# Kernel optimization log

Measured on AMD Instinct MI355X. Metric: run time of the kernel, lower is better.

The kernel has to match this reference:

```python
import jax, jax.numpy as jnp
import numpy as np

B, T, H, V, ADIM, AMAX = 16, 1024, 512, 32000, 512, 10


def setup_inputs() -> dict:
    key = jax.random.key(0)
    ks = jax.random.split(key, 24)
    def n(k, shape, s=0.05):
        return jax.random.normal(k, shape, jnp.float32) * s
    return {
        "instruction": jax.random.randint(ks[0], (B, T), 0, V, dtype=jnp.int32),
        "emb": n(ks[1], (V, H)),
        "wih_f": n(ks[2], (4 * H, H)), "whh_f": n(ks[3], (4 * H, H)),
        "bih_f": n(ks[4], (4 * H,)), "bhh_f": n(ks[5], (4 * H,)),
        "wih_b": n(ks[6], (4 * H, H)), "whh_b": n(ks[7], (4 * H, H)),
        "bih_b": n(ks[8], (4 * H,)), "bhh_b": n(ks[9], (4 * H,)),
        "wg": n(ks[10], (2 * H, 2 * H)), "bg": n(ks[11], (2 * H,)),
        "ws1": n(ks[12], (H, 2 * H)), "bs1": n(ks[13], (H,)),
        "ws2": n(ks[14], (1, H)), "bs2": n(ks[15], (1,)),
        "wd1": n(ks[16], (H, 2 * H)), "bd1": n(ks[17], (H,)),
        "wd2": n(ks[18], (ADIM, H)), "bd2": n(ks[19], (ADIM,)),
        "max_actions": AMAX,
    }


def _lstm(x, wih, whh, bias):
    # x: [B, T, H] -> outputs [B, T, H]; PyTorch gate order i, f, g, o
    h0 = jnp.zeros((x.shape[0], whh.shape[1]), x.dtype)
    def step(carry, xt):
        h, c = carry
        g = xt @ wih.T + h @ whh.T + bias
        i, f, gg, o = jnp.split(g, 4, axis=-1)
        c = jax.nn.sigmoid(f) * c + jax.nn.sigmoid(i) * jnp.tanh(gg)
        h = jax.nn.sigmoid(o) * jnp.tanh(c)
        return (h, c), h
    _, hs = jax.lax.scan(step, (h0, h0), jnp.swapaxes(x, 0, 1))
    return jnp.swapaxes(hs, 0, 1)


def reference(instruction, emb, wih_f, whh_f, bih_f, bhh_f, wih_b, whh_b, bih_b, bhh_b,
              wg, bg, ws1, bs1, ws2, bs2, wd1, bd1, wd2, bd2, max_actions):
    x = emb[instruction]                                   # [B, T, H]
    fwd = _lstm(x, wih_f, whh_f, bih_f + bhh_f)            # [B, T, H]
    bwd = _lstm(x[:, ::-1], wih_b, whh_b, bih_b + bhh_b)[:, ::-1]
    enc = jnp.concatenate([fwd, bwd], axis=-1)             # [B, T, 2H]
    # sequence_lengths=None: h_n[0]=fwd last step, h_n[1]=bwd at t=0
    pooled = jnp.concatenate([fwd[:, -1], bwd[:, 0]], axis=-1)
    gctx = pooled @ wg.T + bg                               # [B, 2H]
    sh = jax.nn.relu(enc @ ws1.T + bs1)
    seg_probs = jax.nn.sigmoid((sh @ ws2.T + bs2)[..., 0])  # [B, T]
    mask = seg_probs > 0.5
    count = mask.sum(axis=-1)
    # first max_actions True positions per row (stable sort keeps time order)
    order = jnp.argsort(jnp.logical_not(mask), axis=1, stable=True)[:, :max_actions]
    gathered = jnp.take_along_axis(enc, order[..., None], axis=1)  # [B, A, 2H]
    slots = jnp.arange(max_actions)
    valid = slots[None, :] < jnp.minimum(count, max_actions)[:, None]
    empty = ((count == 0)[:, None]) & (slots[None, :] == 0)  # fallback: decode global ctx
    dec_in = jnp.where(valid[..., None], gathered, 0.0)
    dec_in = jnp.where(empty[..., None], gctx[:, None, :], dec_in)
    dh = jax.nn.relu(dec_in @ wd1.T + bd1)
    actions = (dh @ wd2.T + bd2) * (valid | empty)[..., None].astype(dec_in.dtype)
    return actions, seg_probs
```

## Files before the change

### kernel.cpp

```cpp
#include <hip/hip_runtime.h>
#include <math.h>

#define T   1024
#define NB  16
#define HD  512

#define OFF_BAR  0
#define OFF_HH   768
#define OFF_SH   (OFF_HH + 16777216)
#define OFF_SEGP (OFF_SH + 8388608)
#define OFF_GCTX (OFF_SEGP + 16384)
#define OFF_SEL  (OFF_GCTX + 16384)

typedef unsigned long long u64;

__device__ __forceinline__ float sigmoidf_(float x){ return 1.0f/(1.0f + __expf(-x)); }
__device__ __forceinline__ float tanhf_(float x){ return 1.0f - 2.0f/(1.0f + __expf(2.0f*x)); }

__global__ __launch_bounds__(256, 2)
void lstm_kernel(const int* __restrict__ instr, const float* __restrict__ emb,
                 const float* __restrict__ wih_f, const float* __restrict__ whh_f,
                 const float* __restrict__ bih_f, const float* __restrict__ bhh_f,
                 const float* __restrict__ wih_b, const float* __restrict__ whh_b,
                 const float* __restrict__ bih_b, const float* __restrict__ bhh_b,
                 float* __restrict__ ws)
{
    float* h_hist = ws + OFF_HH;
    int* flags = (int*)ws;

    const int wg     = blockIdx.x;
    const int dir    = wg >> 8;
    const int rem    = wg & 255;
    const int bgrp   = rem & 3;
    const int uslice = rem >> 2;
    const int U      = uslice * 8;
    const int b0     = bgrp * 4;

    int* barf = flags + (dir*4 + bgrp)*64;

    const float* wih = dir ? wih_b : wih_f;
    const float* whh = dir ? whh_b : whh_f;
    const float* bih = dir ? bih_b : bih_f;
    const float* bhh = dir ? bhh_b : bhh_f;

    const int tid  = threadIdx.x;
    const int wid  = tid >> 6;
    const int lane = tid & 63;

    float wi[64], wh[64];
#pragma unroll
    for (int ri = 0; ri < 8; ++ri){
        int rgl = wid*8 + ri;
        int gate = rgl >> 3, ul = rgl & 7;
        size_t row = (size_t)(gate*HD + U + ul) * HD + lane*8;
        float4 a0 = *(const float4*)(wih + row);
        float4 a1 = *(const float4*)(wih + row + 4);
        float4 b0v = *(const float4*)(whh + row);
        float4 b1v = *(const float4*)(whh + row + 4);
        wi[ri*8+0]=a0.x; wi[ri*8+1]=a0.y; wi[ri*8+2]=a0.z; wi[ri*8+3]=a0.w;
        wi[ri*8+4]=a1.x; wi[ri*8+5]=a1.y; wi[ri*8+6]=a1.z; wi[ri*8+7]=a1.w;
        wh[ri*8+0]=b0v.x; wh[ri*8+1]=b0v.y; wh[ri*8+2]=b0v.z; wh[ri*8+3]=b0v.w;
        wh[ri*8+4]=b1v.x; wh[ri*8+5]=b1v.y; wh[ri*8+6]=b1v.z; wh[ri*8+7]=b1v.w;
    }

    float bI, bF, bG, bO, cst = 0.0f;
    {
        int u = tid & 7;
        bI = bih[0*HD + U + u] + bhh[0*HD + U + u];
        bF = bih[1*HD + U + u] + bhh[1*HD + U + u];
        bG = bih[2*HD + U + u] + bhh[2*HD + U + u];
        bO = bih[3*HD + U + u] + bhh[3*HD + U + u];
    }

    __shared__ float gbuf[128];

    const int jown = ((lane&1)<<4)|((lane&2)<<2)|(lane&4)|((lane&8)>>2)|((lane&16)>>4);
    const int own_bi  = jown >> 3;
    const int own_rgl = wid*8 + (jown & 7);
    const int gslot   = (own_rgl >> 3)*32 + own_bi*8 + (own_rgl & 7);

    for (int s = 0; s < T; ++s){
        const int tp = dir ? (T-1-s) : s;

        float a[32];
#pragma unroll
        for (int j = 0; j < 32; ++j) a[j] = 0.0f;

#pragma unroll
        for (int bi = 0; bi < 4; ++bi){
            int b = b0 + bi;
            int idx = instr[b*T + tp];
            const float* px = emb + (size_t)idx*HD + lane*8;
            float4 x0 = *(const float4*)px;
            float4 x1 = *(const float4*)(px + 4);
            float xs[8] = {x0.x,x0.y,x0.z,x0.w,x1.x,x1.y,x1.z,x1.w};
#pragma unroll
            for (int kk = 0; kk < 8; ++kk){
                float xv = xs[kk];
#pragma unroll
                for (int ri = 0; ri < 8; ++ri)
                    a[bi*8+ri] = fmaf(xv, wi[ri*8+kk], a[bi*8+ri]);
            }
        }

        if (s > 0){
            if (wid == 0){
                for (;;){
                    int v = __hip_atomic_load(barf + lane, __ATOMIC_RELAXED, __HIP_MEMORY_SCOPE_AGENT);
                    if (__all(v >= s)) break;
                    __builtin_amdgcn_s_sleep(1);
                }
            }
            __syncthreads();

            const int tprev = dir ? (T - s) : (s - 1);
            const float* hbase = h_hist + (size_t)(dir*T + tprev)*NB*HD;
#pragma unroll
            for (int bi = 0; bi < 4; ++bi){
                const float* ph = hbase + (size_t)(b0+bi)*HD + lane*8;
                float4 h0 = *(const float4*)ph;
                float4 h1 = *(const float4*)(ph + 4);
                float hs[8] = {h0.x,h0.y,h0.z,h0.w,h1.x,h1.y,h1.z,h1.w};
#pragma unroll
                for (int kk = 0; kk < 8; ++kk){
                    float hv = hs[kk];
#pragma unroll
                    for (int ri = 0; ri < 8; ++ri)
                        a[bi*8+ri] = fmaf(hv, wh[ri*8+kk], a[bi*8+ri]);
                }
            }
        }

#pragma unroll
        for (int m = 0; m < 5; ++m){
            const int half = 16 >> m;
            const bool up = (lane >> m) & 1;
#pragma unroll
            for (int j = 0; j < 16; ++j){
                if (j < half){
                    float lo = a[j], hi = a[j+half];
                    float rlo = __shfl_xor(lo, 1<<m, 64);
                    float rhi = __shfl_xor(hi, 1<<m, 64);
                    a[j] = up ? (hi + rhi) : (lo + rlo);
                }
            }
        }
        a[0] += __shfl_xor(a[0], 32, 64);

        if ((lane & 32) == 0) gbuf[gslot] = a[0];
        __syncthreads();

        if (tid < 32){
            float iv = sigmoidf_(gbuf[      tid] + bI);
            float fv = sigmoidf_(gbuf[ 32 + tid] + bF);
            float gv = tanhf_  (gbuf[ 64 + tid] + bG);
            float ov = sigmoidf_(gbuf[ 96 + tid] + bO);
            cst = fv*cst + iv*gv;
            float hv = ov * tanhf_(cst);
            int b = b0 + (tid >> 3), u = tid & 7;
            __hip_atomic_store(&h_hist[((size_t)(dir*T + tp)*NB + b)*HD + U + u], hv,
                               __ATOMIC_RELAXED, __HIP_MEMORY_SCOPE_AGENT);
        }
        asm volatile("s_waitcnt vmcnt(0)" ::: "memory");
        __builtin_amdgcn_sched_barrier(0);
        if (tid == 0)
            __hip_atomic_store(barf + uslice, s + 1, __ATOMIC_RELAXED, __HIP_MEMORY_SCOPE_AGENT);
    }
}

__global__ __launch_bounds__(256, 2)
void seg_gemm(const float* __restrict__ ws_, const float* __restrict__ ws1,
              const float* __restrict__ bs1)
{
    const float* h_hist = ws_ + OFF_HH;
    float* SH = (float*)(ws_ + OFF_SH);
    __shared__ float As[64][17];
    __shared__ float Bs[64][17];
    const int m0 = blockIdx.x * 64;
    const int n0 = blockIdx.y * 64;
    const int tid = threadIdx.x;
    const int r  = tid >> 2;
    const int kq = (tid & 3) * 4;
    const int ty = tid >> 4, tx = tid & 15;
    const int bI = m0 >> 10;
    const int t0 = m0 & 1023;

    float acc[4][4];
#pragma unroll
    for (int i=0;i<4;i++)
#pragma unroll
        for (int j=0;j<4;j++) acc[i][j]=0.0f;

    for (int kb = 0; kb < 1024; kb += 16){
        int kk = kb + kq;
        const float* ap = (kk < 512)
            ? h_hist + ((size_t)(t0 + r)*NB + bI)*HD + kk
            : h_hist + ((size_t)(T + t0 + r)*NB + bI)*HD + (kk - 512);
        float4 av = *(const float4*)ap;
        As[r][kq+0]=av.x; As[r][kq+1]=av.y; As[r][kq+2]=av.z; As[r][kq+3]=av.w;
        float4 bv = *(const float4*)(ws1 + (size_t)(n0 + r)*1024 + kk);
        Bs[r][kq+0]=bv.x; Bs[r][kq+1]=bv.y; Bs[r][kq+2]=bv.z; Bs[r][kq+3]=bv.w;
        __syncthreads();
#pragma unroll
        for (int k2 = 0; k2 < 16; ++k2){
            float av_[4], bv_[4];
#pragma unroll
            for (int i=0;i<4;i++) av_[i] = As[ty*4+i][k2];
#pragma unroll
            for (int j=0;j<4;j++) bv_[j] = Bs[tx*4+j][k2];
#pragma unroll
            for (int i=0;i<4;i++)
#pragma unroll
                for (int j=0;j<4;j++) acc[i][j] = fmaf(av_[i], bv_[j], acc[i][j]);
        }
        __syncthreads();
    }
#pragma unroll
    for (int i=0;i<4;i++){
        int m = m0 + ty*4 + i;
#pragma unroll
        for (int j=0;j<4;j++){
            int n = n0 + tx*4 + j;
            SH[(size_t)m*512 + n] = fmaxf(acc[i][j] + bs1[n], 0.0f);
        }
    }
}

__global__ void seg_score(const float* __restrict__ ws_, const float* __restrict__ ws2,
                          const float* __restrict__ bs2, float* __restrict__ dout)
{
    const float* SH = ws_ + OFF_SH;
    float* segp = (float*)(ws_ + OFF_SEGP);
    int row  = blockIdx.x*4 + (threadIdx.x >> 6);
    int lane = threadIdx.x & 63;
    const float* p = SH + (size_t)row*512 + lane*8;
    const float* q = ws2 + lane*8;
    float4 a0=*(const float4*)p, a1=*(const float4*)(p+4);
    float4 b0=*(const float4*)q, b1=*(const float4*)(q+4);
    float ssum = a0.x*b0.x + a0.y*b0.y + a0.z*b0.z + a0.w*b0.w
               + a1.x*b1.x + a1.y*b1.y + a1.z*b1.z + a1.w*b1.w;
#pragma unroll
    for (int m=1;m<64;m<<=1) ssum += __shfl_xor(ssum, m, 64);
    if (lane == 0){
        float z = ssum + bs2[0];
        float pr = 1.0f/(1.0f + __expf(-z));
        segp[row] = pr;
        dout[81920 + row] = pr;
    }
}

__global__ void select_gctx(float* __restrict__ ws_, const float* __restrict__ wgm,
                            const float* __restrict__ bgv)
{
    const float* h_hist = ws_ + OFF_HH;
    const float* segp   = ws_ + OFF_SEGP;
    float* gctx = ws_ + OFF_GCTX;
    int* sel = (int*)(ws_ + OFF_SEL);
    int b = blockIdx.x, tid = threadIdx.x;
    __shared__ unsigned char flag[1024];
    __shared__ float pool[1024];
    for (int j = tid; j < 1024; j += 256){
        flag[j] = segp[b*1024 + j] > 0.5f ? 1 : 0;
        pool[j] = (j < 512) ? h_hist[((size_t)1023*NB + b)*HD + j]
                            : h_hist[((size_t)T*NB + b)*HD + (j - 512)];
    }
    __syncthreads();
    if (tid == 0){
        int c = 0;
        int tmp[10];
        for (int j = 0; j < 10; ++j) tmp[j] = 0;
        for (int t = 0; t < 1024; ++t){
            if (flag[t]){ if (c < 10) tmp[c] = t; c++; }
        }
        for (int j = 0; j < 10; ++j) sel[b*12 + j] = tmp[j];
        sel[b*12 + 10] = c;
        sel[b*12 + 11] = 0;
    }
    __syncthreads();
    for (int n = tid; n < 1024; n += 256){
        float acc = bgv[n];
        const float* wr = wgm + (size_t)n*1024;
        for (int k = 0; k < 1024; k += 4){
            acc += wr[k]*pool[k] + wr[k+1]*pool[k+1] + wr[k+2]*pool[k+2] + wr[k+3]*pool[k+3];
        }
        gctx[b*1024 + n] = acc;
    }
}

__global__ void decode(const float* __restrict__ ws_, const float* __restrict__ wd1,
                       const float* __restrict__ bd1, const float* __restrict__ wd2,
                       const float* __restrict__ bd2, float* __restrict__ dout)
{
    const float* h_hist = ws_ + OFF_HH;
    const float* gctx   = ws_ + OFF_GCTX;
    const int* sel = (const int*)(ws_ + OFF_SEL);
    int blk = blockIdx.x;
    int b = blk / 10, slot = blk % 10;
    int tid = threadIdx.x;
    int count = sel[b*12 + 10];
    int nval = count < 10 ? count : 10;
    bool empty = (count == 0);
    float* outp = dout + (size_t)(b*10 + slot)*512;
    if (slot >= nval && !(empty && slot == 0)){
        for (int n = tid; n < 512; n += 256) outp[n] = 0.0f;
        return;
    }
    __shared__ float row[1024];
    __shared__ float dh[512];
    if (empty){
        for (int j = tid; j < 1024; j += 256) row[j] = gctx[b*1024 + j];
    } else {
        int t = sel[b*12 + slot];
        for (int j = tid; j < 1024; j += 256)
            row[j] = (j < 512) ? h_hist[((size_t)t*NB + b)*HD + j]
                               : h_hist[((size_t)(T + t)*NB + b)*HD + (j-512)];
    }
    __syncthreads();
    for (int d = tid; d < 512; d += 256){
        float acc = bd1[d];
        const float* wr = wd1 + (size_t)d*1024;
        for (int k = 0; k < 1024; ++k) acc += wr[k]*row[k];
        dh[d] = fmaxf(acc, 0.0f);
    }
    __syncthreads();
    for (int n = tid; n < 512; n += 256){
        float acc = bd2[n];
        const float* wr = wd2 + (size_t)n*512;
        for (int k = 0; k < 512; ++k) acc += wr[k]*dh[k];
        outp[n] = acc;
    }
}

extern "C" void kernel_launch(void* const* d_in, const int* in_sizes, int n_in,
                              void* d_out, int out_size, void* d_ws, size_t ws_size,
                              hipStream_t stream)
{
    const int*   instr = (const int*)d_in[0];
    const float* emb   = (const float*)d_in[1];
    const float* wih_f = (const float*)d_in[2];
    const float* whh_f = (const float*)d_in[3];
    const float* bih_f = (const float*)d_in[4];
    const float* bhh_f = (const float*)d_in[5];
    const float* wih_b = (const float*)d_in[6];
    const float* whh_b = (const float*)d_in[7];
    const float* bih_b = (const float*)d_in[8];
    const float* bhh_b = (const float*)d_in[9];
    const float* wg_   = (const float*)d_in[10];
    const float* bg_   = (const float*)d_in[11];
    const float* ws1   = (const float*)d_in[12];
    const float* bs1   = (const float*)d_in[13];
    const float* ws2   = (const float*)d_in[14];
    const float* bs2   = (const float*)d_in[15];
    const float* wd1   = (const float*)d_in[16];
    const float* bd1   = (const float*)d_in[17];
    const float* wd2   = (const float*)d_in[18];
    const float* bd2   = (const float*)d_in[19];
    float* out = (float*)d_out;
    float* ws  = (float*)d_ws;

    hipMemsetAsync(d_ws, 0, 2048, stream);

    hipLaunchKernelGGL(lstm_kernel, dim3(512), dim3(256), 0, stream,
                       instr, emb, wih_f, whh_f, bih_f, bhh_f,
                       wih_b, whh_b, bih_b, bhh_b, ws);
    hipLaunchKernelGGL(seg_gemm, dim3(256, 8), dim3(256), 0, stream, ws, ws1, bs1);
    hipLaunchKernelGGL(seg_score, dim3(4096), dim3(256), 0, stream, ws, ws2, bs2, out);
    hipLaunchKernelGGL(select_gctx, dim3(16), dim3(256), 0, stream, ws, wg_, bg_);
    hipLaunchKernelGGL(decode, dim3(160), dim3(256), 0, stream, ws, wd1, bd1, wd2, bd2, out);
}
```

Measured before the change: 4.421 ms.

## Fuse segment score projection into seg GEMM epilogue and transpose LDS tiles

```diff
diff --git a/kernel.cpp b/kernel.cpp
--- a/kernel.cpp
+++ b/kernel.cpp
@@ -7,8 +7,8 @@
 
 #define OFF_BAR  0
 #define OFF_HH   768
-#define OFF_SH   (OFF_HH + 16777216)
-#define OFF_SEGP (OFF_SH + 8388608)
+#define OFF_SCR  (OFF_HH + 16777216)
+#define OFF_SEGP (OFF_SCR + 16384)
 #define OFF_GCTX (OFF_SEGP + 16384)
 #define OFF_SEL  (OFF_GCTX + 16384)
 
@@ -170,12 +170,12 @@
 
 __global__ __launch_bounds__(256, 2)
 void seg_gemm(const float* __restrict__ ws_, const float* __restrict__ ws1,
-              const float* __restrict__ bs1)
+              const float* __restrict__ bs1, const float* __restrict__ ws2)
 {
     const float* h_hist = ws_ + OFF_HH;
-    float* SH = (float*)(ws_ + OFF_SH);
-    __shared__ float As[64][17];
-    __shared__ float Bs[64][17];
+    float* scores = (float*)(ws_ + OFF_SCR);
+    __shared__ float As[16][68];
+    __shared__ float Bs[16][68];
     const int m0 = blockIdx.x * 64;
     const int n0 = blockIdx.y * 64;
     const int tid = threadIdx.x;
@@ -197,56 +197,54 @@
             ? h_hist + ((size_t)(t0 + r)*NB + bI)*HD + kk
             : h_hist + ((size_t)(T + t0 + r)*NB + bI)*HD + (kk - 512);
         float4 av = *(const float4*)ap;
-        As[r][kq+0]=av.x; As[r][kq+1]=av.y; As[r][kq+2]=av.z; As[r][kq+3]=av.w;
+        As[kq+0][r]=av.x; As[kq+1][r]=av.y; As[kq+2][r]=av.z; As[kq+3][r]=av.w;
         float4 bv = *(const float4*)(ws1 + (size_t)(n0 + r)*1024 + kk);
-        Bs[r][kq+0]=bv.x; Bs[r][kq+1]=bv.y; Bs[r][kq+2]=bv.z; Bs[r][kq+3]=bv.w;
+        Bs[kq+0][r]=bv.x; Bs[kq+1][r]=bv.y; Bs[kq+2][r]=bv.z; Bs[kq+3][r]=bv.w;
         __syncthreads();
 #pragma unroll
         for (int k2 = 0; k2 < 16; ++k2){
-            float av_[4], bv_[4];
-#pragma unroll
-            for (int i=0;i<4;i++) av_[i] = As[ty*4+i][k2];
-#pragma unroll
-            for (int j=0;j<4;j++) bv_[j] = Bs[tx*4+j][k2];
+            float4 av_ = *(const float4*)&As[k2][ty*4];
+            float4 bv_ = *(const float4*)&Bs[k2][tx*4];
+            float am[4] = {av_.x, av_.y, av_.z, av_.w};
+            float bn[4] = {bv_.x, bv_.y, bv_.z, bv_.w};
 #pragma unroll
             for (int i=0;i<4;i++)
 #pragma unroll
-                for (int j=0;j<4;j++) acc[i][j] = fmaf(av_[i], bv_[j], acc[i][j]);
+                for (int j=0;j<4;j++) acc[i][j] = fmaf(am[i], bn[j], acc[i][j]);
         }
         __syncthreads();
     }
+
+    float b1[4], w2[4];
+#pragma unroll
+    for (int j=0;j<4;j++){
+        int n = n0 + tx*4 + j;
+        b1[j] = bs1[n];
+        w2[j] = ws2[n];
+    }
 #pragma unroll
     for (int i=0;i<4;i++){
-        int m = m0 + ty*4 + i;
-#pragma unroll
-        for (int j=0;j<4;j++){
-            int n = n0 + tx*4 + j;
-            SH[(size_t)m*512 + n] = fmaxf(acc[i][j] + bs1[n], 0.0f);
-        }
-    }
-}
-
-__global__ void seg_score(const float* __restrict__ ws_, const float* __restrict__ ws2,
-                          const float* __restrict__ bs2, float* __restrict__ dout)
-{
-    const float* SH = ws_ + OFF_SH;
-    float* segp = (float*)(ws_ + OFF_SEGP);
-    int row  = blockIdx.x*4 + (threadIdx.x >> 6);
-    int lane = threadIdx.x & 63;
-    const float* p = SH + (size_t)row*512 + lane*8;
-    const float* q = ws2 + lane*8;
-    float4 a0=*(const float4*)p, a1=*(const float4*)(p+4);
-    float4 b0=*(const float4*)q, b1=*(const float4*)(q+4);
-    float ssum = a0.x*b0.x + a0.y*b0.y + a0.z*b0.z + a0.w*b0.w
-               + a1.x*b1.x + a1.y*b1.y + a1.z*b1.z + a1.w*b1.w;
-#pragma unroll
-    for (int m=1;m<64;m<<=1) ssum += __shfl_xor(ssum, m, 64);
-    if (lane == 0){
-        float z = ssum + bs2[0];
-        float pr = 1.0f/(1.0f + __expf(-z));
-        segp[row] = pr;
-        dout[81920 + row] = pr;
-    }
+        float partial = 0.0f;
+#pragma unroll
+        for (int j=0;j<4;j++)
+            partial += fmaxf(acc[i][j] + b1[j], 0.0f) * w2[j];
+#pragma unroll
+        for (int mm = 1; mm < 16; mm <<= 1)
+            partial += __shfl_xor(partial, mm, 64);
+        if (tx == 0)
+            atomicAdd(&scores[m0 + ty*4 + i], partial);
+    }
+}
+
+__global__ void seg_final(float* __restrict__ ws_, const float* __restrict__ bs2,
+                          float* __restrict__ dout)
+{
+    const float* scores = ws_ + OFF_SCR;
+    float* segp = ws_ + OFF_SEGP;
+    int m = blockIdx.x*256 + threadIdx.x;
+    float pr = 1.0f/(1.0f + __expf(-(scores[m] + bs2[0])));
+    segp[m] = pr;
+    dout[81920 + m] = pr;
 }
 
 __global__ void select_gctx(float* __restrict__ ws_, const float* __restrict__ wgm,
@@ -359,12 +357,13 @@
     float* ws  = (float*)d_ws;
 
     hipMemsetAsync(d_ws, 0, 2048, stream);
+    hipMemsetAsync((char*)d_ws + (size_t)OFF_SCR*4, 0, 16384*4, stream);
 
     hipLaunchKernelGGL(lstm_kernel, dim3(512), dim3(256), 0, stream,
                        instr, emb, wih_f, whh_f, bih_f, bhh_f,
                        wih_b, whh_b, bih_b, bhh_b, ws);
-    hipLaunchKernelGGL(seg_gemm, dim3(256, 8), dim3(256), 0, stream, ws, ws1, bs1);
-    hipLaunchKernelGGL(seg_score, dim3(4096), dim3(256), 0, stream, ws, ws2, bs2, out);
+    hipLaunchKernelGGL(seg_gemm, dim3(256, 8), dim3(256), 0, stream, ws, ws1, bs1, ws2);
+    hipLaunchKernelGGL(seg_final, dim3(64), dim3(256), 0, stream, ws, bs2, out);
     hipLaunchKernelGGL(select_gctx, dim3(16), dim3(256), 0, stream, ws, wg_, bg_);
     hipLaunchKernelGGL(decode, dim3(160), dim3(256), 0, stream, ws, wd1, bd1, wd2, bd2, out);
 }
```

Result: faster. 4.295 ms (-2.8%).
